# Kernel optimization log

Hardware: AMD Instinct MI355X
Metric: run time of the kernel (lower is better)

## Reference

```python
import jax, jax.numpy as jnp
import numpy as np

B, T, D_MODEL, HEAD_DIM = 8, 2048, 1024, 128


def setup_inputs() -> dict:
    key = jax.random.key(0)
    k1, k2, k3, k4 = jax.random.split(key, 4)
    scale = 1.0 / np.sqrt(D_MODEL)
    return {
        "x": jax.random.normal(k1, (B, T, D_MODEL), dtype=jnp.float32),
        "Wq": jax.random.normal(k2, (HEAD_DIM, D_MODEL), dtype=jnp.float32) * scale,
        "Wk": jax.random.normal(k3, (HEAD_DIM, D_MODEL), dtype=jnp.float32) * scale,
        "Wv": jax.random.normal(k4, (HEAD_DIM, D_MODEL), dtype=jnp.float32) * scale,
    }


def reference(x, Wq, Wk, Wv) -> jnp.ndarray:
    # x: [B, T, C]; torch Linear(no bias): y = x @ W.T, W: [head_dim, d_model]
    q = jnp.einsum("btc,hc->bth", x, Wq)  # [B, T, H]
    k = jnp.einsum("btc,hc->bth", x, Wk)
    v = jnp.einsum("btc,hc->bth", x, Wv)
    head_dim = Wq.shape[0]
    scores = jnp.einsum("bqh,bkh->bqk", q, k) / jnp.sqrt(jnp.float32(head_dim))  # [B, T, T]
    T_ = x.shape[1]
    causal = jnp.tril(jnp.ones((T_, T_), dtype=bool))
    scores = jnp.where(causal, scores, -jnp.inf)
    probs = jax.nn.softmax(scores, axis=-1)
    # dropout is identity at inference (eval mode)
    out = jnp.einsum("bqk,bkh->bqh", probs, v)  # [B, T, head_dim]
    return out
```

## Files before the change

kernel.cpp:

```cpp
#include <hip/hip_runtime.h>
#include <math.h>

#define T_ 2048
#define C_ 1024
#define H_ 128
#define NB 8
#define XN 16777216
#define WN 131072
#define SC 0.08838834764831845f

typedef __attribute__((ext_vector_type(8))) short bf16x8;
typedef __attribute__((ext_vector_type(8))) unsigned short u16x8;
typedef __attribute__((ext_vector_type(4))) float f32x4;

#define MFMA16(a,b,c) __builtin_amdgcn_mfma_f32_16x16x32_bf16((a),(b),(c),0,0,0)

__device__ __forceinline__ unsigned short f2bf(float f) {
    union { float f; unsigned u; } v; v.f = f;
    unsigned r = v.u + 0x7fffu + ((v.u >> 16) & 1u);
    return (unsigned short)(r >> 16);
}
__device__ __forceinline__ float bf2f(unsigned short u) {
    union { unsigned u; float f; } v; v.u = ((unsigned)u) << 16; return v.f;
}
__device__ __forceinline__ void gld16(void* lds, const void* g) {
    __builtin_amdgcn_global_load_lds(
        (const __attribute__((address_space(1))) unsigned*)g,
        (__attribute__((address_space(3))) unsigned*)lds, 16, 0, 0);
}

__global__ __launch_bounds__(256) void xwconv(const float* __restrict__ x,
                                              const float* __restrict__ Wq,
                                              const float* __restrict__ Wk,
                                              const float* __restrict__ Wv,
                                              unsigned short* __restrict__ xb,
                                              unsigned short* __restrict__ Wb) {
    long e = ((long)blockIdx.x * 256 + threadIdx.x) * 8;
    u16x8 o;
    if (e < XN) {
        const float4* p = (const float4*)(x + e);
        float4 a = p[0], b = p[1];
        o[0]=f2bf(a.x); o[1]=f2bf(a.y); o[2]=f2bf(a.z); o[3]=f2bf(a.w);
        o[4]=f2bf(b.x); o[5]=f2bf(b.y); o[6]=f2bf(b.z); o[7]=f2bf(b.w);
        *(u16x8*)(xb + e) = o;
    } else {
        long j = e - XN;
        int which = (int)(j >> 17);
        long off = j & (WN - 1);
        const float* src = (which == 0) ? Wq : (which == 1 ? Wk : Wv);
        float s = (which == 0) ? SC : 1.0f;
        const float4* p = (const float4*)(src + off);
        float4 a = p[0], b = p[1];
        o[0]=f2bf(a.x*s); o[1]=f2bf(a.y*s); o[2]=f2bf(a.z*s); o[3]=f2bf(a.w*s);
        o[4]=f2bf(b.x*s); o[5]=f2bf(b.y*s); o[6]=f2bf(b.z*s); o[7]=f2bf(b.w*s);
        *(u16x8*)(Wb + j) = o;
    }
}

__global__ __launch_bounds__(256) void proj(const unsigned short* __restrict__ xb,
                                            const unsigned short* __restrict__ Wb,
                                            unsigned short* __restrict__ Q,
                                            unsigned short* __restrict__ K,
                                            unsigned short* __restrict__ V) {
    __shared__ unsigned short Xs[128][32];
    __shared__ unsigned short Ws[128][32];
    const int tid = threadIdx.x, wave = tid >> 6, lane = tid & 63;
    const int quad = lane >> 4, l16 = lane & 15;
    const int m0 = blockIdx.x * 128, n0 = blockIdx.y;
    const int wm = wave >> 1, wn = wave & 1;

    f32x4 acc[4][4];
    #pragma unroll
    for (int i = 0; i < 4; i++)
        #pragma unroll
        for (int j = 0; j < 4; j++) acc[i][j] = {0.f, 0.f, 0.f, 0.f};

    const unsigned short* xg = xb + (size_t)(m0 + wave * 32 + (lane >> 2)) * C_ + (lane & 3) * 8;
    const unsigned short* wg = Wb + (size_t)(n0 * 128 + wave * 32 + (lane >> 2)) * C_ + (lane & 3) * 8;

    for (int kc = 0; kc < C_; kc += 32) {
        gld16(&Xs[wave * 32][0],      xg + kc);
        gld16(&Xs[wave * 32 + 16][0], xg + kc + 16 * C_);
        gld16(&Ws[wave * 32][0],      wg + kc);
        gld16(&Ws[wave * 32 + 16][0], wg + kc + 16 * C_);
        __syncthreads();
        bf16x8 af[4], bfr[4];
        #pragma unroll
        for (int mf = 0; mf < 4; mf++) af[mf]  = *(bf16x8*)&Xs[wm * 64 + mf * 16 + l16][quad * 8];
        #pragma unroll
        for (int nf = 0; nf < 4; nf++) bfr[nf] = *(bf16x8*)&Ws[wn * 64 + nf * 16 + l16][quad * 8];
        #pragma unroll
        for (int mf = 0; mf < 4; mf++)
            #pragma unroll
            for (int nf = 0; nf < 4; nf++)
                acc[mf][nf] = MFMA16(af[mf], bfr[nf], acc[mf][nf]);
        __syncthreads();
    }

    unsigned short* dst = (n0 == 0) ? Q : (n0 == 1 ? K : V);
    #pragma unroll
    for (int mf = 0; mf < 4; mf++)
        #pragma unroll
        for (int nf = 0; nf < 4; nf++)
            #pragma unroll
            for (int r = 0; r < 4; r++)
                dst[(size_t)(m0 + wm * 64 + mf * 16 + quad * 4 + r) * H_ + wn * 64 + nf * 16 + l16]
                    = f2bf(acc[mf][nf][r]);
}

__global__ __launch_bounds__(256) void attn(const unsigned short* __restrict__ Qg,
                                            const unsigned short* __restrict__ Kg,
                                            const unsigned short* __restrict__ Vg,
                                            unsigned short* __restrict__ Ob,
                                            float* __restrict__ Ml) {
    const int qt = blockIdx.x, b = blockIdx.y, s = blockIdx.z;
    const int qbase = qt * 64, kstart = s * 512;
    if (kstart >= qbase + 64) return;
    const int kend  = (kstart + 512 < qbase + 64) ? kstart + 512 : qbase + 64;
    const int niter = (kend - kstart) >> 6;

    __shared__ unsigned short Qs[4][64][32];
    __shared__ unsigned short Ks[4][64][32];
    __shared__ unsigned short Vt[128 * 64];
    __shared__ unsigned short Ps[4][16][72];

    const int tid = threadIdx.x, wave = tid >> 6, lane = tid & 63;
    const int quad = lane >> 4, l16 = lane & 15;
    const size_t base = (size_t)b * T_ * H_;

    const unsigned short* qsrc = Qg + base + (size_t)(qbase + (lane >> 2)) * H_ + wave * 32 + (lane & 3) * 8;
    const unsigned short* ksrc = Kg + base + (size_t)(kstart + (lane >> 2)) * H_ + wave * 32 + (lane & 3) * 8;
    #pragma unroll
    for (int p = 0; p < 4; p++) gld16(&Qs[wave][p * 16][0], qsrc + (size_t)p * 16 * H_);
    #pragma unroll
    for (int p = 0; p < 4; p++) gld16(&Ks[wave][p * 16][0], ksrc + (size_t)p * 16 * H_);

    const unsigned short* vsrc = Vg + base + (size_t)(kstart + wave * 8 + quad * 2) * H_ + l16 * 8;
    u16x8 vr[2][2];
    vr[0][0] = *(const u16x8*)vsrc;             vr[0][1] = *(const u16x8*)(vsrc + H_);
    vr[1][0] = *(const u16x8*)(vsrc + 32 * H_); vr[1][1] = *(const u16x8*)(vsrc + 33 * H_);

    f32x4 o[8];
    #pragma unroll
    for (int i = 0; i < 8; i++) o[i] = {0.f, 0.f, 0.f, 0.f};
    float m_i[4], l_i[4];
    #pragma unroll
    for (int r = 0; r < 4; r++) { m_i[r] = -INFINITY; l_i[r] = 0.f; }

    __syncthreads();

    {
        #pragma unroll
        for (int g = 0; g < 2; g++) {
            int t0 = wave * 8 + g * 32 + quad * 2;
            int t8 = t0 >> 3;
            #pragma unroll
            for (int j = 0; j < 8; j++) {
                int h = l16 * 8 + j;
                unsigned pk = (unsigned)vr[g][0][j] | ((unsigned)vr[g][1][j] << 16);
                int blk = (t8 ^ (h & 7) ^ ((h >> 3) & 7)) & 7;
                *(unsigned*)&Vt[h * 64 + blk * 8 + (t0 & 7)] = pk;
            }
        }
    }

    bf16x8 qf[4];
    #pragma unroll
    for (int kk = 0; kk < 4; kk++) qf[kk] = *(bf16x8*)&Qs[kk][wave * 16 + l16][quad * 8];

    const int qloc = wave * 16 + quad * 4;

    for (int kt = 0; ; kt++) {
        const int kbase = kstart + kt * 64;
        f32x4 sf[4];
        #pragma unroll
        for (int nf = 0; nf < 4; nf++) sf[nf] = {0.f, 0.f, 0.f, 0.f};
        #pragma unroll
        for (int kk = 0; kk < 4; kk++)
            #pragma unroll
            for (int nf = 0; nf < 4; nf++) {
                bf16x8 bfr = *(bf16x8*)&Ks[kk][nf * 16 + l16][quad * 8];
                sf[nf] = MFMA16(qf[kk], bfr, sf[nf]);
            }
        if (kbase == qbase) {
            #pragma unroll
            for (int nf = 0; nf < 4; nf++) {
                int kloc = nf * 16 + l16;
                #pragma unroll
                for (int r = 0; r < 4; r++)
                    if (kloc > qloc + r) sf[nf][r] = -INFINITY;
            }
        }
        float alpha[4];
        #pragma unroll
        for (int r = 0; r < 4; r++) {
            float v = fmaxf(fmaxf(sf[0][r], sf[1][r]), fmaxf(sf[2][r], sf[3][r]));
            v = fmaxf(v, __shfl_xor(v, 1, 64));
            v = fmaxf(v, __shfl_xor(v, 2, 64));
            v = fmaxf(v, __shfl_xor(v, 4, 64));
            v = fmaxf(v, __shfl_xor(v, 8, 64));
            float mnew = fmaxf(m_i[r], v);
            alpha[r] = __expf(m_i[r] - mnew);
            m_i[r] = mnew;
        }
        #pragma unroll
        for (int r = 0; r < 4; r++) {
            float rs = 0.f;
            #pragma unroll
            for (int nf = 0; nf < 4; nf++) {
                float e = __expf(sf[nf][r] - m_i[r]);
                sf[nf][r] = e; rs += e;
            }
            rs += __shfl_xor(rs, 1, 64);
            rs += __shfl_xor(rs, 2, 64);
            rs += __shfl_xor(rs, 4, 64);
            rs += __shfl_xor(rs, 8, 64);
            l_i[r] = alpha[r] * l_i[r] + rs;
        }
        #pragma unroll
        for (int nf = 0; nf < 4; nf++)
            #pragma unroll
            for (int r = 0; r < 4; r++)
                Ps[wave][quad * 4 + r][nf * 16 + l16] = f2bf(sf[nf][r]);
        #pragma unroll
        for (int i = 0; i < 8; i++) {
            o[i][0] *= alpha[0]; o[i][1] *= alpha[1];
            o[i][2] *= alpha[2]; o[i][3] *= alpha[3];
        }
        __syncthreads();

        const bool more = (kt + 1 < niter);
        if (more) {
            ksrc += 64 * H_;
            #pragma unroll
            for (int p = 0; p < 4; p++) gld16(&Ks[wave][p * 16][0], ksrc + (size_t)p * 16 * H_);
            vsrc += 64 * H_;
            vr[0][0] = *(const u16x8*)vsrc;             vr[0][1] = *(const u16x8*)(vsrc + H_);
            vr[1][0] = *(const u16x8*)(vsrc + 32 * H_); vr[1][1] = *(const u16x8*)(vsrc + 33 * H_);
        }
        bf16x8 pa0 = *(bf16x8*)&Ps[wave][l16][quad * 8];
        bf16x8 pa1 = *(bf16x8*)&Ps[wave][l16][32 + quad * 8];
        #pragma unroll
        for (int nf = 0; nf < 8; nf++) {
            int h = nf * 16 + l16;
            int ex = (h & 7) ^ ((h >> 3) & 7);
            bf16x8 v0 = *(bf16x8*)&Vt[h * 64 + ((quad ^ ex) & 7) * 8];
            bf16x8 v1 = *(bf16x8*)&Vt[h * 64 + (((quad + 4) ^ ex) & 7) * 8];
            o[nf] = MFMA16(pa0, v0, o[nf]);
            o[nf] = MFMA16(pa1, v1, o[nf]);
        }
        if (!more) break;
        __syncthreads();
        #pragma unroll
        for (int g = 0; g < 2; g++) {
            int t0 = wave * 8 + g * 32 + quad * 2;
            int t8 = t0 >> 3;
            #pragma unroll
            for (int j = 0; j < 8; j++) {
                int h = l16 * 8 + j;
                unsigned pk = (unsigned)vr[g][0][j] | ((unsigned)vr[g][1][j] << 16);
                int blk = (t8 ^ (h & 7) ^ ((h >> 3) & 7)) & 7;
                *(unsigned*)&Vt[h * 64 + blk * 8 + (t0 & 7)] = pk;
            }
        }
    }

    const size_t obase = ((size_t)((qt * 8 + b) * 4 + s)) * 64 * 128;
    #pragma unroll
    for (int r = 0; r < 4; r++) {
        float invl = 1.0f / l_i[r];
        #pragma unroll
        for (int nf = 0; nf < 8; nf++)
            Ob[obase + (size_t)(qloc + r) * 128 + nf * 16 + l16] = f2bf(o[nf][r] * invl);
    }
    if (l16 == 0) {
        int ridx = ((qt * 8 + b) * 4 + s) * 64 + qloc;
        #pragma unroll
        for (int r = 0; r < 4; r++) { Ml[(ridx + r) * 2] = m_i[r]; Ml[(ridx + r) * 2 + 1] = l_i[r]; }
    }
}

__global__ __launch_bounds__(256) void merge(const unsigned short* __restrict__ Ob,
                                             const float* __restrict__ Ml,
                                             float* __restrict__ out) {
    const int qt = blockIdx.x, b = blockIdx.y;
    const int ns = (qt >> 3) + 1;
    const int tid = threadIdx.x;
    const int row = tid >> 2, c0 = (tid & 3) * 32;
    const int pb = (qt * 8 + b) * 4;

    float mv[4], lv[4], mg = -INFINITY;
    for (int s2 = 0; s2 < ns; s2++) {
        mv[s2] = Ml[((pb + s2) * 64 + row) * 2];
        lv[s2] = Ml[((pb + s2) * 64 + row) * 2 + 1];
        mg = fmaxf(mg, mv[s2]);
    }
    float L = 0.f, w[4];
    for (int s2 = 0; s2 < ns; s2++) { w[s2] = lv[s2] * __expf(mv[s2] - mg); L += w[s2]; }
    float inv = 1.0f / L;

    float accv[32];
    #pragma unroll
    for (int i = 0; i < 32; i++) accv[i] = 0.f;
    for (int s2 = 0; s2 < ns; s2++) {
        const unsigned short* op = Ob + ((size_t)((pb + s2) * 64 + row)) * 128 + c0;
        #pragma unroll
        for (int cc = 0; cc < 4; cc++) {
            u16x8 v = *(const u16x8*)(op + cc * 8);
            #pragma unroll
            for (int j = 0; j < 8; j++) accv[cc * 8 + j] += w[s2] * bf2f(v[j]);
        }
    }
    float* od = out + ((size_t)(b * T_ + qt * 64 + row)) * 128 + c0;
    #pragma unroll
    for (int cc = 0; cc < 8; cc++) {
        float4 w4 = { accv[cc*4] * inv, accv[cc*4+1] * inv, accv[cc*4+2] * inv, accv[cc*4+3] * inv };
        *(float4*)(od + cc * 4) = w4;
    }
}

extern "C" void kernel_launch(void* const* d_in, const int* in_sizes, int n_in,
                              void* d_out, int out_size, void* d_ws, size_t ws_size,
                              hipStream_t stream) {
    const float* x  = (const float*)d_in[0];
    const float* Wq = (const float*)d_in[1];
    const float* Wk = (const float*)d_in[2];
    const float* Wv = (const float*)d_in[3];

    char* ws = (char*)d_ws;
    unsigned short* Wb = (unsigned short*)ws;
    unsigned short* xb = (unsigned short*)(ws + (size_t)(1u << 20));
    unsigned short* Ob = (unsigned short*)(ws + (size_t)(1u << 20));
    float*          Ml = (float*)(ws + (size_t)18 * (1u << 20));
    unsigned short* Q  = (unsigned short*)(ws + (size_t)34 * (1u << 20));
    unsigned short* K  = Q + (size_t)16384 * 128;
    unsigned short* V  = K + (size_t)16384 * 128;
    float* out = (float*)d_out;

    hipLaunchKernelGGL(xwconv, dim3(8384), dim3(256), 0, stream, x, Wq, Wk, Wv, xb, Wb);
    hipLaunchKernelGGL(proj,   dim3(128, 3), dim3(256), 0, stream, xb, Wb, Q, K, V);
    hipLaunchKernelGGL(attn,   dim3(32, NB, 4), dim3(256), 0, stream, Q, K, V, Ob, Ml);
    hipLaunchKernelGGL(merge,  dim3(32, NB), dim3(256), 0, stream, Ob, Ml, out);
}
```

Measured before the change: 182.7 us.

## Fuse x conversion into fused QKV projection and rework split-K attention

Removes the separate fp32-to-bf16 pass over x: the projection now reads fp32 x directly, converts it in registers and computes Q, K and V together in one double-buffered GEMM over 64-row tiles. This avoids writing and re-reading a 32MB intermediate. Attention splits keys into 256-wide chunks instead of 512, schedules the longest query tiles first, computes the transposed score so each lane owns one query row, swizzles the P buffer, and loads Q straight into registers. The merge kernel uses a compact slot layout. Risks: the projection grid shrinks to 256 blocks with one block per SM, and more splits mean more merge traffic.

```diff
diff --git a/kernel.cpp b/kernel.cpp
--- a/kernel.cpp
+++ b/kernel.cpp
@@ -1,11 +1,11 @@
 #include <hip/hip_runtime.h>
+#include <hip/hip_bf16.h>
 #include <math.h>
 
 #define T_ 2048
 #define C_ 1024
 #define H_ 128
 #define NB 8
-#define XN 16777216
 #define WN 131072
 #define SC 0.08838834764831845f
 
@@ -23,209 +23,219 @@
 __device__ __forceinline__ float bf2f(unsigned short u) {
     union { unsigned u; float f; } v; v.u = ((unsigned)u) << 16; return v.f;
 }
+__device__ __forceinline__ unsigned pk2bf(float a, float b) {
+    __hip_bfloat162 h = __float22bfloat162_rn(float2{a, b});
+    union { __hip_bfloat162 h; unsigned u; } v; v.h = h; return v.u;
+}
 __device__ __forceinline__ void gld16(void* lds, const void* g) {
     __builtin_amdgcn_global_load_lds(
         (const __attribute__((address_space(1))) unsigned*)g,
         (__attribute__((address_space(3))) unsigned*)lds, 16, 0, 0);
 }
 
-__global__ __launch_bounds__(256) void xwconv(const float* __restrict__ x,
-                                              const float* __restrict__ Wq,
-                                              const float* __restrict__ Wk,
-                                              const float* __restrict__ Wv,
-                                              unsigned short* __restrict__ xb,
-                                              unsigned short* __restrict__ Wb) {
-    long e = ((long)blockIdx.x * 256 + threadIdx.x) * 8;
-    u16x8 o;
-    if (e < XN) {
-        const float4* p = (const float4*)(x + e);
-        float4 a = p[0], b = p[1];
-        o[0]=f2bf(a.x); o[1]=f2bf(a.y); o[2]=f2bf(a.z); o[3]=f2bf(a.w);
-        o[4]=f2bf(b.x); o[5]=f2bf(b.y); o[6]=f2bf(b.z); o[7]=f2bf(b.w);
-        *(u16x8*)(xb + e) = o;
-    } else {
-        long j = e - XN;
-        int which = (int)(j >> 17);
-        long off = j & (WN - 1);
-        const float* src = (which == 0) ? Wq : (which == 1 ? Wk : Wv);
-        float s = (which == 0) ? SC : 1.0f;
-        const float4* p = (const float4*)(src + off);
-        float4 a = p[0], b = p[1];
-        o[0]=f2bf(a.x*s); o[1]=f2bf(a.y*s); o[2]=f2bf(a.z*s); o[3]=f2bf(a.w*s);
-        o[4]=f2bf(b.x*s); o[5]=f2bf(b.y*s); o[6]=f2bf(b.z*s); o[7]=f2bf(b.w*s);
-        *(u16x8*)(Wb + j) = o;
-    }
-}
-
-__global__ __launch_bounds__(256) void proj(const unsigned short* __restrict__ xb,
-                                            const unsigned short* __restrict__ Wb,
-                                            unsigned short* __restrict__ Q,
-                                            unsigned short* __restrict__ K,
-                                            unsigned short* __restrict__ V) {
-    __shared__ unsigned short Xs[128][32];
-    __shared__ unsigned short Ws[128][32];
-    const int tid = threadIdx.x, wave = tid >> 6, lane = tid & 63;
+__global__ __launch_bounds__(256) void wconv(const float* __restrict__ Wq,
+                                             const float* __restrict__ Wk,
+                                             const float* __restrict__ Wv,
+                                             unsigned short* __restrict__ Wb) {
+    int e = (blockIdx.x * 256 + threadIdx.x) * 8;
+    int which = e >> 17;
+    int off = e & (WN - 1);
+    const float* src = (which == 0) ? Wq : (which == 1 ? Wk : Wv);
+    float s = (which == 0) ? SC : 1.0f;
+    const float4* p = (const float4*)(src + off);
+    float4 a = p[0], b = p[1];
+    uint4 o = { pk2bf(a.x * s, a.y * s), pk2bf(a.z * s, a.w * s),
+                pk2bf(b.x * s, b.y * s), pk2bf(b.z * s, b.w * s) };
+    *(uint4*)(Wb + e) = o;
+}
+
+__global__ __launch_bounds__(256, 1) void proj(const float* __restrict__ x,
+                                               const unsigned short* __restrict__ Wb,
+                                               unsigned short* __restrict__ Q,
+                                               unsigned short* __restrict__ K,
+                                               unsigned short* __restrict__ V) {
+    __shared__ unsigned short Xs[2][2][64][40];
+    __shared__ unsigned short Ws[2][2][384][32];
+
+    const int tid  = threadIdx.x;
+    const int wave = tid >> 6, lane = tid & 63;
     const int quad = lane >> 4, l16 = lane & 15;
-    const int m0 = blockIdx.x * 128, n0 = blockIdx.y;
-    const int wm = wave >> 1, wn = wave & 1;
-
-    f32x4 acc[4][4];
+    const int m0   = blockIdx.x * 64;
+
+    f32x4 acc[4][6];
     #pragma unroll
     for (int i = 0; i < 4; i++)
         #pragma unroll
-        for (int j = 0; j < 4; j++) acc[i][j] = {0.f, 0.f, 0.f, 0.f};
-
-    const unsigned short* xg = xb + (size_t)(m0 + wave * 32 + (lane >> 2)) * C_ + (lane & 3) * 8;
-    const unsigned short* wg = Wb + (size_t)(n0 * 128 + wave * 32 + (lane >> 2)) * C_ + (lane & 3) * 8;
-
-    for (int kc = 0; kc < C_; kc += 32) {
-        gld16(&Xs[wave * 32][0],      xg + kc);
-        gld16(&Xs[wave * 32 + 16][0], xg + kc + 16 * C_);
-        gld16(&Ws[wave * 32][0],      wg + kc);
-        gld16(&Ws[wave * 32 + 16][0], wg + kc + 16 * C_);
+        for (int j = 0; j < 6; j++) acc[i][j] = {0.f, 0.f, 0.f, 0.f};
+
+    const int xrow = tid >> 2, xcg = tid & 3;
+    const int xck = xcg >> 1, xco = (xcg & 1) * 16;
+    const float* xg = x + (size_t)(m0 + xrow) * C_ + xcg * 16;
+    const unsigned short* wg = Wb + (size_t)(wave * 96 + (lane >> 2)) * C_ + (lane & 3) * 8;
+
+    #define STAGE(buf, kc) do {                                                   \
+        _Pragma("unroll")                                                         \
+        for (int kkc = 0; kkc < 2; kkc++)                                         \
+            _Pragma("unroll")                                                     \
+            for (int rb = 0; rb < 6; rb++)                                        \
+                gld16(&Ws[buf][kkc][wave * 96 + rb * 16][0],                      \
+                      wg + (size_t)rb * 16 * C_ + (kc) + kkc * 32);               \
+        const float* xp = xg + (kc);                                              \
+        float4 f0 = *(const float4*)xp,      f1 = *(const float4*)(xp + 4);       \
+        float4 f2 = *(const float4*)(xp + 8), f3 = *(const float4*)(xp + 12);     \
+        uint4 u0 = { pk2bf(f0.x,f0.y), pk2bf(f0.z,f0.w),                          \
+                     pk2bf(f1.x,f1.y), pk2bf(f1.z,f1.w) };                        \
+        uint4 u1 = { pk2bf(f2.x,f2.y), pk2bf(f2.z,f2.w),                          \
+                     pk2bf(f3.x,f3.y), pk2bf(f3.z,f3.w) };                        \
+        *(uint4*)&Xs[buf][xck][xrow][xco]     = u0;                               \
+        *(uint4*)&Xs[buf][xck][xrow][xco + 8] = u1;                               \
+    } while (0)
+
+    STAGE(0, 0);
+    for (int it = 0; it < 16; it++) {
         __syncthreads();
-        bf16x8 af[4], bfr[4];
-        #pragma unroll
-        for (int mf = 0; mf < 4; mf++) af[mf]  = *(bf16x8*)&Xs[wm * 64 + mf * 16 + l16][quad * 8];
-        #pragma unroll
-        for (int nf = 0; nf < 4; nf++) bfr[nf] = *(bf16x8*)&Ws[wn * 64 + nf * 16 + l16][quad * 8];
+        if (it < 15) { STAGE((it + 1) & 1, (it + 1) * 64); }
+        const int buf = it & 1;
+        bf16x8 af[4][2];
+        #pragma unroll
+        for (int kk = 0; kk < 2; kk++)
+            #pragma unroll
+            for (int mf = 0; mf < 4; mf++)
+                af[mf][kk] = *(bf16x8*)&Xs[buf][kk][mf * 16 + l16][quad * 8];
+        #pragma unroll
+        for (int kk = 0; kk < 2; kk++)
+            #pragma unroll
+            for (int nf = 0; nf < 6; nf++) {
+                bf16x8 bq = *(bf16x8*)&Ws[buf][kk][wave * 96 + nf * 16 + l16][quad * 8];
+                #pragma unroll
+                for (int mf = 0; mf < 4; mf++)
+                    acc[mf][nf] = MFMA16(af[mf][kk], bq, acc[mf][nf]);
+            }
+    }
+    #undef STAGE
+
+    #pragma unroll
+    for (int nf = 0; nf < 6; nf++) {
+        int nb = wave * 96 + nf * 16;
+        int which = nb >> 7;
+        unsigned short* dst = (which == 0) ? Q : (which == 1 ? K : V);
+        int c = (nb & 127) + l16;
         #pragma unroll
         for (int mf = 0; mf < 4; mf++)
             #pragma unroll
-            for (int nf = 0; nf < 4; nf++)
-                acc[mf][nf] = MFMA16(af[mf], bfr[nf], acc[mf][nf]);
-        __syncthreads();
-    }
-
-    unsigned short* dst = (n0 == 0) ? Q : (n0 == 1 ? K : V);
-    #pragma unroll
-    for (int mf = 0; mf < 4; mf++)
-        #pragma unroll
-        for (int nf = 0; nf < 4; nf++)
-            #pragma unroll
             for (int r = 0; r < 4; r++)
-                dst[(size_t)(m0 + wm * 64 + mf * 16 + quad * 4 + r) * H_ + wn * 64 + nf * 16 + l16]
-                    = f2bf(acc[mf][nf][r]);
-}
-
-__global__ __launch_bounds__(256) void attn(const unsigned short* __restrict__ Qg,
-                                            const unsigned short* __restrict__ Kg,
-                                            const unsigned short* __restrict__ Vg,
-                                            unsigned short* __restrict__ Ob,
-                                            float* __restrict__ Ml) {
-    const int qt = blockIdx.x, b = blockIdx.y, s = blockIdx.z;
-    const int qbase = qt * 64, kstart = s * 512;
-    if (kstart >= qbase + 64) return;
-    const int kend  = (kstart + 512 < qbase + 64) ? kstart + 512 : qbase + 64;
+                dst[(size_t)(m0 + mf * 16 + quad * 4 + r) * H_ + c] = f2bf(acc[mf][nf][r]);
+    }
+}
+
+__global__ __launch_bounds__(256, 3) void attn(const unsigned short* __restrict__ Qg,
+                                               const unsigned short* __restrict__ Kg,
+                                               const unsigned short* __restrict__ Vg,
+                                               unsigned short* __restrict__ Ob,
+                                               float* __restrict__ Ml) {
+    const int bx = blockIdx.x;
+    const int s  = bx & 7, qt = 31 - (bx >> 3);
+    const int b  = blockIdx.y;
+    const int qbase = qt * 64, kstart = s * 256;
+    if (kstart > qbase) return;
+    const int kend  = (kstart + 256 < qbase + 64) ? kstart + 256 : qbase + 64;
     const int niter = (kend - kstart) >> 6;
 
-    __shared__ unsigned short Qs[4][64][32];
     __shared__ unsigned short Ks[4][64][32];
     __shared__ unsigned short Vt[128 * 64];
-    __shared__ unsigned short Ps[4][16][72];
+    __shared__ unsigned short Ps[4][16][64];
 
     const int tid = threadIdx.x, wave = tid >> 6, lane = tid & 63;
     const int quad = lane >> 4, l16 = lane & 15;
     const size_t base = (size_t)b * T_ * H_;
 
-    const unsigned short* qsrc = Qg + base + (size_t)(qbase + (lane >> 2)) * H_ + wave * 32 + (lane & 3) * 8;
     const unsigned short* ksrc = Kg + base + (size_t)(kstart + (lane >> 2)) * H_ + wave * 32 + (lane & 3) * 8;
     #pragma unroll
-    for (int p = 0; p < 4; p++) gld16(&Qs[wave][p * 16][0], qsrc + (size_t)p * 16 * H_);
-    #pragma unroll
     for (int p = 0; p < 4; p++) gld16(&Ks[wave][p * 16][0], ksrc + (size_t)p * 16 * H_);
-
     const unsigned short* vsrc = Vg + base + (size_t)(kstart + wave * 8 + quad * 2) * H_ + l16 * 8;
     u16x8 vr[2][2];
     vr[0][0] = *(const u16x8*)vsrc;             vr[0][1] = *(const u16x8*)(vsrc + H_);
     vr[1][0] = *(const u16x8*)(vsrc + 32 * H_); vr[1][1] = *(const u16x8*)(vsrc + 33 * H_);
 
+    bf16x8 qf[4];
+    const unsigned short* qp = Qg + base + (size_t)(qbase + wave * 16 + l16) * H_ + quad * 8;
+    #pragma unroll
+    for (int kk = 0; kk < 4; kk++) qf[kk] = *(const bf16x8*)(qp + kk * 32);
+
     f32x4 o[8];
     #pragma unroll
     for (int i = 0; i < 8; i++) o[i] = {0.f, 0.f, 0.f, 0.f};
-    float m_i[4], l_i[4];
-    #pragma unroll
-    for (int r = 0; r < 4; r++) { m_i[r] = -INFINITY; l_i[r] = 0.f; }
+    float m_i = -INFINITY, l_i = 0.f;
+    const int swz = (l16 & 7) << 3;
+    const int qg = qbase + wave * 16 + l16;
 
     __syncthreads();
 
-    {
-        #pragma unroll
-        for (int g = 0; g < 2; g++) {
-            int t0 = wave * 8 + g * 32 + quad * 2;
-            int t8 = t0 >> 3;
-            #pragma unroll
-            for (int j = 0; j < 8; j++) {
-                int h = l16 * 8 + j;
-                unsigned pk = (unsigned)vr[g][0][j] | ((unsigned)vr[g][1][j] << 16);
-                int blk = (t8 ^ (h & 7) ^ ((h >> 3) & 7)) & 7;
-                *(unsigned*)&Vt[h * 64 + blk * 8 + (t0 & 7)] = pk;
-            }
-        }
-    }
-
-    bf16x8 qf[4];
-    #pragma unroll
-    for (int kk = 0; kk < 4; kk++) qf[kk] = *(bf16x8*)&Qs[kk][wave * 16 + l16][quad * 8];
-
-    const int qloc = wave * 16 + quad * 4;
+    #pragma unroll
+    for (int g = 0; g < 2; g++) {
+        int t0 = wave * 8 + g * 32 + quad * 2;
+        int t8 = t0 >> 3;
+        #pragma unroll
+        for (int j = 0; j < 8; j++) {
+            int h = l16 * 8 + j;
+            unsigned pk = (unsigned)(unsigned short)vr[g][0][j] | ((unsigned)(unsigned short)vr[g][1][j] << 16);
+            int blk = (t8 ^ (h & 7) ^ ((h >> 3) & 7)) & 7;
+            *(unsigned*)&Vt[h * 64 + blk * 8 + (t0 & 7)] = pk;
+        }
+    }
 
     for (int kt = 0; ; kt++) {
         const int kbase = kstart + kt * 64;
-        f32x4 sf[4];
-        #pragma unroll
-        for (int nf = 0; nf < 4; nf++) sf[nf] = {0.f, 0.f, 0.f, 0.f};
+        f32x4 st[4];
+        #pragma unroll
+        for (int nf = 0; nf < 4; nf++) st[nf] = {0.f, 0.f, 0.f, 0.f};
         #pragma unroll
         for (int kk = 0; kk < 4; kk++)
             #pragma unroll
             for (int nf = 0; nf < 4; nf++) {
-                bf16x8 bfr = *(bf16x8*)&Ks[kk][nf * 16 + l16][quad * 8];
-                sf[nf] = MFMA16(qf[kk], bfr, sf[nf]);
-            }
-        if (kbase == qbase) {
+                bf16x8 kfr = *(bf16x8*)&Ks[kk][nf * 16 + l16][quad * 8];
+                st[nf] = MFMA16(kfr, qf[kk], st[nf]);
+            }
+        if (kbase + 64 > qbase) {
             #pragma unroll
             for (int nf = 0; nf < 4; nf++) {
-                int kloc = nf * 16 + l16;
+                int kg = kbase + nf * 16 + quad * 4;
                 #pragma unroll
                 for (int r = 0; r < 4; r++)
-                    if (kloc > qloc + r) sf[nf][r] = -INFINITY;
-            }
-        }
-        float alpha[4];
-        #pragma unroll
-        for (int r = 0; r < 4; r++) {
-            float v = fmaxf(fmaxf(sf[0][r], sf[1][r]), fmaxf(sf[2][r], sf[3][r]));
-            v = fmaxf(v, __shfl_xor(v, 1, 64));
-            v = fmaxf(v, __shfl_xor(v, 2, 64));
-            v = fmaxf(v, __shfl_xor(v, 4, 64));
-            v = fmaxf(v, __shfl_xor(v, 8, 64));
-            float mnew = fmaxf(m_i[r], v);
-            alpha[r] = __expf(m_i[r] - mnew);
-            m_i[r] = mnew;
-        }
-        #pragma unroll
-        for (int r = 0; r < 4; r++) {
-            float rs = 0.f;
-            #pragma unroll
-            for (int nf = 0; nf < 4; nf++) {
-                float e = __expf(sf[nf][r] - m_i[r]);
-                sf[nf][r] = e; rs += e;
-            }
-            rs += __shfl_xor(rs, 1, 64);
-            rs += __shfl_xor(rs, 2, 64);
-            rs += __shfl_xor(rs, 4, 64);
-            rs += __shfl_xor(rs, 8, 64);
-            l_i[r] = alpha[r] * l_i[r] + rs;
-        }
+                    if (kg + r > qg) st[nf][r] = -INFINITY;
+            }
+        }
+        float mx = st[0][0];
         #pragma unroll
         for (int nf = 0; nf < 4; nf++)
             #pragma unroll
-            for (int r = 0; r < 4; r++)
-                Ps[wave][quad * 4 + r][nf * 16 + l16] = f2bf(sf[nf][r]);
+            for (int r = 0; r < 4; r++) mx = fmaxf(mx, st[nf][r]);
+        mx = fmaxf(mx, __shfl_xor(mx, 16, 64));
+        mx = fmaxf(mx, __shfl_xor(mx, 32, 64));
+        float mnew = fmaxf(m_i, mx);
+        float al = __expf(m_i - mnew);
+        m_i = mnew;
+        float rs = 0.f;
+        #pragma unroll
+        for (int nf = 0; nf < 4; nf++)
+            #pragma unroll
+            for (int r = 0; r < 4; r++) {
+                float e = __expf(st[nf][r] - mnew);
+                st[nf][r] = e; rs += e;
+            }
+        rs += __shfl_xor(rs, 16, 64);
+        rs += __shfl_xor(rs, 32, 64);
+        l_i = al * l_i + rs;
+        #pragma unroll
+        for (int nf = 0; nf < 4; nf++) {
+            uint2 pk = { pk2bf(st[nf][0], st[nf][1]), pk2bf(st[nf][2], st[nf][3]) };
+            *(uint2*)&Ps[wave][l16][(nf * 16 + quad * 4) ^ swz] = pk;
+        }
+        float a0 = __shfl(al, quad * 4 + 0, 64), a1 = __shfl(al, quad * 4 + 1, 64);
+        float a2 = __shfl(al, quad * 4 + 2, 64), a3 = __shfl(al, quad * 4 + 3, 64);
         #pragma unroll
         for (int i = 0; i < 8; i++) {
-            o[i][0] *= alpha[0]; o[i][1] *= alpha[1];
-            o[i][2] *= alpha[2]; o[i][3] *= alpha[3];
+            o[i][0] *= a0; o[i][1] *= a1; o[i][2] *= a2; o[i][3] *= a3;
         }
         __syncthreads();
 
@@ -238,8 +248,8 @@
             vr[0][0] = *(const u16x8*)vsrc;             vr[0][1] = *(const u16x8*)(vsrc + H_);
             vr[1][0] = *(const u16x8*)(vsrc + 32 * H_); vr[1][1] = *(const u16x8*)(vsrc + 33 * H_);
         }
-        bf16x8 pa0 = *(bf16x8*)&Ps[wave][l16][quad * 8];
-        bf16x8 pa1 = *(bf16x8*)&Ps[wave][l16][32 + quad * 8];
+        bf16x8 pa0 = *(bf16x8*)&Ps[wave][l16][(quad * 8) ^ swz];
+        bf16x8 pa1 = *(bf16x8*)&Ps[wave][l16][(32 + quad * 8) ^ swz];
         #pragma unroll
         for (int nf = 0; nf < 8; nf++) {
             int h = nf * 16 + l16;
@@ -258,25 +268,31 @@
             #pragma unroll
             for (int j = 0; j < 8; j++) {
                 int h = l16 * 8 + j;
-                unsigned pk = (unsigned)vr[g][0][j] | ((unsigned)vr[g][1][j] << 16);
+                unsigned pk = (unsigned)(unsigned short)vr[g][0][j] | ((unsigned)(unsigned short)vr[g][1][j] << 16);
                 int blk = (t8 ^ (h & 7) ^ ((h >> 3) & 7)) & 7;
                 *(unsigned*)&Vt[h * 64 + blk * 8 + (t0 & 7)] = pk;
             }
         }
     }
 
-    const size_t obase = ((size_t)((qt * 8 + b) * 4 + s)) * 64 * 128;
+    const int g2 = qt >> 2;
+    const int Pq = 2 * g2 * (g2 + 1) + (qt & 3) * (g2 + 1);
+    const int slot = (Pq + s) * NB + b;
+    float lq[4];
+    #pragma unroll
+    for (int r = 0; r < 4; r++) lq[r] = __shfl(l_i, quad * 4 + r, 64);
+    const size_t obase = (size_t)slot * 64 * 128;
     #pragma unroll
     for (int r = 0; r < 4; r++) {
-        float invl = 1.0f / l_i[r];
+        float invl = 1.0f / lq[r];
         #pragma unroll
         for (int nf = 0; nf < 8; nf++)
-            Ob[obase + (size_t)(qloc + r) * 128 + nf * 16 + l16] = f2bf(o[nf][r] * invl);
-    }
-    if (l16 == 0) {
-        int ridx = ((qt * 8 + b) * 4 + s) * 64 + qloc;
-        #pragma unroll
-        for (int r = 0; r < 4; r++) { Ml[(ridx + r) * 2] = m_i[r]; Ml[(ridx + r) * 2 + 1] = l_i[r]; }
+            Ob[obase + (size_t)(wave * 16 + quad * 4 + r) * 128 + nf * 16 + l16] = f2bf(o[nf][r] * invl);
+    }
+    if (lane < 16) {
+        int ridx = slot * 64 + wave * 16 + l16;
+        Ml[ridx * 2]     = m_i;
+        Ml[ridx * 2 + 1] = l_i;
     }
 }
 
@@ -284,18 +300,20 @@
                                              const float* __restrict__ Ml,
                                              float* __restrict__ out) {
     const int qt = blockIdx.x, b = blockIdx.y;
-    const int ns = (qt >> 3) + 1;
+    const int g = qt >> 2;
+    const int Pq = 2 * g * (g + 1) + (qt & 3) * (g + 1);
+    const int ns = g + 1;
     const int tid = threadIdx.x;
     const int row = tid >> 2, c0 = (tid & 3) * 32;
-    const int pb = (qt * 8 + b) * 4;
-
-    float mv[4], lv[4], mg = -INFINITY;
+
+    float mv[8], lv[8], mg = -INFINITY;
     for (int s2 = 0; s2 < ns; s2++) {
-        mv[s2] = Ml[((pb + s2) * 64 + row) * 2];
-        lv[s2] = Ml[((pb + s2) * 64 + row) * 2 + 1];
+        int slot = (Pq + s2) * NB + b;
+        mv[s2] = Ml[(slot * 64 + row) * 2];
+        lv[s2] = Ml[(slot * 64 + row) * 2 + 1];
         mg = fmaxf(mg, mv[s2]);
     }
-    float L = 0.f, w[4];
+    float L = 0.f, w[8];
     for (int s2 = 0; s2 < ns; s2++) { w[s2] = lv[s2] * __expf(mv[s2] - mg); L += w[s2]; }
     float inv = 1.0f / L;
 
@@ -303,7 +321,8 @@
     #pragma unroll
     for (int i = 0; i < 32; i++) accv[i] = 0.f;
     for (int s2 = 0; s2 < ns; s2++) {
-        const unsigned short* op = Ob + ((size_t)((pb + s2) * 64 + row)) * 128 + c0;
+        int slot = (Pq + s2) * NB + b;
+        const unsigned short* op = Ob + ((size_t)(slot * 64 + row)) * 128 + c0;
         #pragma unroll
         for (int cc = 0; cc < 4; cc++) {
             u16x8 v = *(const u16x8*)(op + cc * 8);
@@ -329,16 +348,15 @@
 
     char* ws = (char*)d_ws;
     unsigned short* Wb = (unsigned short*)ws;
-    unsigned short* xb = (unsigned short*)(ws + (size_t)(1u << 20));
-    unsigned short* Ob = (unsigned short*)(ws + (size_t)(1u << 20));
-    float*          Ml = (float*)(ws + (size_t)18 * (1u << 20));
-    unsigned short* Q  = (unsigned short*)(ws + (size_t)34 * (1u << 20));
-    unsigned short* K  = Q + (size_t)16384 * 128;
-    unsigned short* V  = K + (size_t)16384 * 128;
+    unsigned short* Q  = (unsigned short*)(ws + (size_t) 1 * (1u << 20));
+    unsigned short* K  = (unsigned short*)(ws + (size_t) 5 * (1u << 20));
+    unsigned short* V  = (unsigned short*)(ws + (size_t) 9 * (1u << 20));
+    unsigned short* Ob = (unsigned short*)(ws + (size_t)13 * (1u << 20));
+    float*          Ml = (float*)(ws + (size_t)32 * (1u << 20));
     float* out = (float*)d_out;
 
-    hipLaunchKernelGGL(xwconv, dim3(8384), dim3(256), 0, stream, x, Wq, Wk, Wv, xb, Wb);
-    hipLaunchKernelGGL(proj,   dim3(128, 3), dim3(256), 0, stream, xb, Wb, Q, K, V);
-    hipLaunchKernelGGL(attn,   dim3(32, NB, 4), dim3(256), 0, stream, Q, K, V, Ob, Ml);
-    hipLaunchKernelGGL(merge,  dim3(32, NB), dim3(256), 0, stream, Ob, Ml, out);
-}
+    hipLaunchKernelGGL(wconv, dim3(192), dim3(256), 0, stream, Wq, Wk, Wv, Wb);
+    hipLaunchKernelGGL(proj,  dim3(256), dim3(256), 0, stream, x, Wb, Q, K, V);
+    hipLaunchKernelGGL(attn,  dim3(256, NB), dim3(256), 0, stream, Q, K, V, Ob, Ml);
+    hipLaunchKernelGGL(merge, dim3(32, NB), dim3(256), 0, stream, Ob, Ml, out);
+}
```

After: 173.8 us. -4.8%, faster.
